# Kernel optimization log

Hardware: AMD Instinct MI355X
Metric: run time of the kernel (lower is better)

Reference implementation:

```python
import jax, jax.numpy as jnp
import numpy as np

B, P = 512, 256          # batch, n_assets
MAX_W = 0.1              # max_weight from __init__
EPS = 1e-8               # config.EPSILON
N_PGD = 250              # projected-gradient iterations (QP solve)
N_BISECT = 30            # bisection iterations for simplex projection
N_POWER = 20             # power iterations for spectral norm


def setup_inputs() -> dict:
    key = jax.random.key(0)
    k1, k2 = jax.random.split(key, 2)
    A = jax.random.normal(k1, (B, P, P), jnp.float32)
    # PSD covariance, as required by cp.Parameter(PSD=True)
    sigma = jnp.einsum('bij,bkj->bik', A, A) / P + 1e-3 * jnp.eye(P, dtype=jnp.float32)
    beta = jax.random.uniform(k2, (B, P), jnp.float32)  # nonneg risk budgets
    w_prev = jnp.full((B, P), 1.0 / P, jnp.float32)     # default equal weight
    return {
        'sigma': sigma,
        'beta': beta,
        'w_prev': w_prev,
        'log_lambda1': jnp.float32(-3.0),
        'log_lambda2': jnp.float32(-2.0),
    }


def _project_capped_simplex(v, c):
    """Euclidean projection onto {w : sum w = 1, 0 <= w <= c}, batched over leading dims.
    Solves sum(clip(v - tau, 0, c)) = 1 for tau by bisection (monotone decreasing)."""
    lo = v.min(-1, keepdims=True) - c
    hi = v.max(-1, keepdims=True)

    def body(i, carry):
        lo, hi = carry
        tau = 0.5 * (lo + hi)
        s = jnp.clip(v - tau, 0.0, c).sum(-1, keepdims=True)
        too_big = s > 1.0
        return (jnp.where(too_big, tau, lo), jnp.where(too_big, hi, tau))

    lo, hi = jax.lax.fori_loop(0, N_BISECT, body, (lo, hi))
    tau = 0.5 * (lo + hi)
    return jnp.clip(v - tau, 0.0, c)


def _solve_qp(sigma, beta, w_prev, lam1, lam2):
    """min_w  w'Pw - beta'w + lam1*||w||_1 + lam2*||w - w_prev||^2
       s.t.   sum w = 1, 0 <= w <= MAX_W
    via projected gradient descent (on the feasible set w>=0, ||w||_1 = sum w,
    so lam1 contributes a constant lam1 to the gradient)."""
    # step size 1/L with L = 2*lambda_max(P) + 2*lam2, estimated by power iteration
    S = jax.lax.stop_gradient(sigma)
    v = jnp.full((B, P), 1.0 / np.sqrt(P), sigma.dtype)

    def pbody(i, v):
        u = jnp.einsum('bij,bj->bi', S, v)
        return u / (jnp.linalg.norm(u, axis=-1, keepdims=True) + EPS)

    v = jax.lax.fori_loop(0, N_POWER, pbody, v)
    lmax = jnp.einsum('bi,bij,bj->b', v, S, v)                    # [B]
    step = jax.lax.stop_gradient(1.0 / (2.0 * lmax + 2.0 * lam2 + 1e-6))  # [B]

    w0 = jnp.full((B, P), 1.0 / P, sigma.dtype)

    def pgd(w, _):
        g = (2.0 * jnp.einsum('bij,bj->bi', sigma, w)
             - beta + lam1 + 2.0 * lam2 * (w - w_prev))
        w = _project_capped_simplex(w - step[:, None] * g, MAX_W)
        return w, None

    w, _ = jax.lax.scan(pgd, w0, None, length=N_PGD)
    return w


def reference(sigma, beta, w_prev, log_lambda1, log_lambda2):
    lam1 = jnp.exp(log_lambda1)
    lam2 = jnp.exp(log_lambda2)
    w = _solve_qp(sigma, beta, w_prev, lam1, lam2)
    # post-processing from forward(): clamp then renormalize
    w = jnp.clip(w, 0.0, MAX_W)
    return w / (w.sum(-1, keepdims=True) + EPS)
```

## Files before the change

### kernel.cpp

```cpp
#include <hip/hip_runtime.h>
#include <math.h>


#define PP    256
#define MAXW  0.1f
#define EPSF  1e-8f
#define NPGD  250
#define NPOW  20
#define NILLMAX 10
#define FTOL  4e-6f
#define STOPTOL 1e-7f
#define MINIT 48

#define R3S   272
#define TJS   68
#define WRDS  72
#define VCOPY 280

typedef float v2 __attribute__((ext_vector_type(2)));
typedef float v4t __attribute__((ext_vector_type(4)));

template<int CTRL>
__device__ __forceinline__ float dpp_zero(float x) {
    return __int_as_float(__builtin_amdgcn_update_dpp(
        0, __float_as_int(x), CTRL, 0xF, 0xF, true));
}
template<int CTRL>
__device__ __forceinline__ float dpp_keep(float x) {
    int xi = __float_as_int(x);
    return __int_as_float(__builtin_amdgcn_update_dpp(xi, xi, CTRL, 0xF, 0xF, false));
}
__device__ __forceinline__ float rdlane63(float x) {
    return __int_as_float(__builtin_amdgcn_readlane(__float_as_int(x), 63));
}
__device__ __forceinline__ float wave_sum63(float s) {
    s += dpp_zero<0x111>(s);
    s += dpp_zero<0x112>(s);
    s += dpp_zero<0x114>(s);
    s += dpp_zero<0x118>(s);
    s += dpp_zero<0x142>(s);
    s += dpp_zero<0x143>(s);
    return s;
}
__device__ __forceinline__ float wave_min63(float m) {
    m = fminf(m, dpp_keep<0x111>(m));
    m = fminf(m, dpp_keep<0x112>(m));
    m = fminf(m, dpp_keep<0x114>(m));
    m = fminf(m, dpp_keep<0x118>(m));
    m = fminf(m, dpp_keep<0x142>(m));
    m = fminf(m, dpp_keep<0x143>(m));
    return m;
}
__device__ __forceinline__ float wave_max63(float m) {
    m = fmaxf(m, dpp_keep<0x111>(m));
    m = fmaxf(m, dpp_keep<0x112>(m));
    m = fmaxf(m, dpp_keep<0x114>(m));
    m = fmaxf(m, dpp_keep<0x118>(m));
    m = fmaxf(m, dpp_keep<0x142>(m));
    m = fmaxf(m, dpp_keep<0x143>(m));
    return m;
}

__global__ __launch_bounds__(256, 2)
__attribute__((amdgpu_waves_per_eu(2, 2)))
void drb_kernel(const float* __restrict__ sigma,
                const float* __restrict__ beta,
                const float* __restrict__ wprev,
                const float* __restrict__ pl1,
                const float* __restrict__ pl2,
                float* __restrict__ out)
{
    const int b    = blockIdx.x;
    const int tid  = threadIdx.x;
    const int lane = tid & 63;
    const int wv   = tid >> 6;
    const int ti   = tid >> 2;
    const int tj   = tid & 3;

    __shared__ __align__(16) float sigR3[64 * R3S];
    __shared__ __align__(16) float wcop[4 * VCOPY];
    __shared__ __align__(16) float stage[2][256];

    const float* Sb = sigma + (size_t)b * (PP * PP);

    v2 s0[32], s1[32], s2[32];
    {
        const float* r0 = Sb + (4 * ti + 0) * PP + 64 * tj;
#pragma unroll
        for (int k = 0; k < 16; ++k) {
            v4t t = *(const v4t*)(r0 + 4 * k);
            s0[2*k]   = __builtin_shufflevector(t, t, 0, 1);
            s0[2*k+1] = __builtin_shufflevector(t, t, 2, 3);
        }
    }
    {
        const float* r1 = Sb + (4 * ti + 1) * PP + 64 * tj;
#pragma unroll
        for (int k = 0; k < 16; ++k) {
            v4t t = *(const v4t*)(r1 + 4 * k);
            s1[2*k]   = __builtin_shufflevector(t, t, 0, 1);
            s1[2*k+1] = __builtin_shufflevector(t, t, 2, 3);
        }
    }
    {
        const float* r2 = Sb + (4 * ti + 2) * PP + 64 * tj;
#pragma unroll
        for (int k = 0; k < 16; ++k) {
            v4t t = *(const v4t*)(r2 + 4 * k);
            s2[2*k]   = __builtin_shufflevector(t, t, 0, 1);
            s2[2*k+1] = __builtin_shufflevector(t, t, 2, 3);
        }
    }
    {
        const float* r3 = Sb + (4 * ti + 3) * PP + 64 * tj;
        float* d3 = sigR3 + ti * R3S + TJS * tj;
#pragma unroll
        for (int k = 0; k < 16; ++k)
            *(v4t*)(d3 + 4 * k) = *(const v4t*)(r3 + 4 * k);
    }

    const float bt   = beta[b * PP + tid];
    const float wp   = wprev[b * PP + tid];
    const float lam1 = expf(pl1[0]);
    const float lam2 = expf(pl2[0]);

    float* wme = wcop + wv * VCOPY;
    const int wst = 4 * lane + 8 * (lane >> 4);
    const float* wrd = wme + WRDS * tj;

    auto matvec = [&]() -> float {
        v2 y0a = {0.f, 0.f}, y0b = {0.f, 0.f};
        v2 y1a = {0.f, 0.f}, y1b = {0.f, 0.f};
        v2 y2a = {0.f, 0.f}, y2b = {0.f, 0.f};
        v2 y3a = {0.f, 0.f}, y3b = {0.f, 0.f};
        const float* p3 = sigR3 + ti * R3S + TJS * tj;
#pragma unroll
        for (int k = 0; k < 16; ++k) {
            v4t wq = *(const v4t*)(wrd + 4 * k);
            v2 w01 = __builtin_shufflevector(wq, wq, 0, 1);
            v2 w23 = __builtin_shufflevector(wq, wq, 2, 3);
            y0a = __builtin_elementwise_fma(s0[2*k],   w01, y0a);
            y0b = __builtin_elementwise_fma(s0[2*k+1], w23, y0b);
            y1a = __builtin_elementwise_fma(s1[2*k],   w01, y1a);
            y1b = __builtin_elementwise_fma(s1[2*k+1], w23, y1b);
            y2a = __builtin_elementwise_fma(s2[2*k],   w01, y2a);
            y2b = __builtin_elementwise_fma(s2[2*k+1], w23, y2b);
            v4t q = *(const v4t*)(p3 + 4 * k);
            v2 q01 = __builtin_shufflevector(q, q, 0, 1);
            v2 q23 = __builtin_shufflevector(q, q, 2, 3);
            y3a = __builtin_elementwise_fma(q01, w01, y3a);
            y3b = __builtin_elementwise_fma(q23, w23, y3b);
        }
        float r0 = (y0a.x + y0a.y) + (y0b.x + y0b.y);
        float r1 = (y1a.x + y1a.y) + (y1b.x + y1b.y);
        float r2 = (y2a.x + y2a.y) + (y2b.x + y2b.y);
        float r3 = (y3a.x + y3a.y) + (y3b.x + y3b.y);
        r0 += dpp_zero<0x4E>(r0); r1 += dpp_zero<0x4E>(r1);
        r2 += dpp_zero<0x4E>(r2); r3 += dpp_zero<0x4E>(r3);
        r0 += dpp_zero<0xB1>(r0); r1 += dpp_zero<0xB1>(r1);
        r2 += dpp_zero<0xB1>(r2); r3 += dpp_zero<0xB1>(r3);
        float a01 = (tj & 1) ? r1 : r0;
        float a23 = (tj & 1) ? r3 : r2;
        return (tj & 2) ? a23 : a01;
    };

    {
        v4t c = {0.0625f, 0.0625f, 0.0625f, 0.0625f};
        *(v4t*)(wme + wst) = c;
    }

    float y_last = 0.f, a_last = 1.f;
#pragma unroll 1
    for (int pi = 0; pi < NPOW; ++pi) {
        float y = matvec();
        stage[pi & 1][tid] = y;
        __syncthreads();
        v4t u4 = *(const v4t*)(&stage[pi & 1][4 * lane]);
        float ss = fmaf(u4.x, u4.x, fmaf(u4.y, u4.y, fmaf(u4.z, u4.z, u4.w * u4.w)));
        float a  = 1.f / (sqrtf(rdlane63(wave_sum63(ss))) + EPSF);
        v4t n4 = {a * u4.x, a * u4.y, a * u4.z, a * u4.w};
        *(v4t*)(wme + wst) = n4;
        y_last = y; a_last = a;
    }

    float stepf;
    {
        float ysv = matvec();
        float p   = (a_last * y_last) * ysv;
        stage[0][tid] = p;
        __syncthreads();
        v4t p4 = *(const v4t*)(&stage[0][4 * lane]);
        float lmax = rdlane63(wave_sum63((p4.x + p4.y) + (p4.z + p4.w)));
        stepf = 1.f / (2.f * lmax + 2.f * lam2 + 1e-6f);
        __syncthreads();
    }

    float w_own = 1.f / 256.f;
    {
        v4t c = {1.f/256.f, 1.f/256.f, 1.f/256.f, 1.f/256.f};
        *(v4t*)(wme + wst) = c;
    }
    const float Ac = 1.f - 2.f * lam2 * stepf;
    const float Bc = -2.f * stepf;
    const float Cc = stepf * (bt - lam1 + 2.f * lam2 * wp);

    float tau_pred = 0.f;
    float tau_last = 0.f;
    float dtau_last = 0.f;

    v4t w4_prev = {1.f/256.f, 1.f/256.f, 1.f/256.f, 1.f/256.f};
    float dm1 = 1.f, dm2 = 1.f;

#pragma unroll 1
    for (int it = 0; it < NPGD; ++it) {
        if (it >= MINIT && dm1 < STOPTOL && dm2 < STOPTOL) break;

        float y = matvec();
        float v_own = fmaf(w_own, Ac, fmaf(y, Bc, Cc));
        const int sb = it & 1;
        stage[sb][tid] = v_own;
        __syncthreads();

        __builtin_amdgcn_s_setprio(1);
        v4t v4 = *(const v4t*)(&stage[sb][4 * lane]);

        float tau = tau_pred;
        {
            float d0 = v4.x - tau, d1 = v4.y - tau;
            float d2 = v4.z - tau, d3 = v4.w - tau;
            float c0 = __builtin_amdgcn_fmed3f(d0, 0.f, MAXW);
            float c1 = __builtin_amdgcn_fmed3f(d1, 0.f, MAXW);
            float c2 = __builtin_amdgcn_fmed3f(d2, 0.f, MAXW);
            float c3 = __builtin_amdgcn_fmed3f(d3, 0.f, MAXW);
            float Sw = wave_sum63((c0 + c1) + (c2 + c3));
            float f  = rdlane63(Sw) - 1.f;

            if (!(fabsf(f) <= FTOL)) {
                float mnl = fminf(fminf(v4.x, v4.y), fminf(v4.z, v4.w));
                float mxl = fmaxf(fmaxf(v4.x, v4.y), fmaxf(v4.z, v4.w));
                float n0 = ((d0 > 0.f) & (d0 < MAXW)) ? 1.f : 0.f;
                float n1 = ((d1 > 0.f) & (d1 < MAXW)) ? 1.f : 0.f;
                float n2 = ((d2 > 0.f) & (d2 < MAXW)) ? 1.f : 0.f;
                float n3 = ((d3 > 0.f) & (d3 < MAXW)) ? 1.f : 0.f;
                float mnw = wave_min63(mnl);
                float mxw = wave_max63(mxl);
                float Nw  = wave_sum63((n0 + n1) + (n2 + n3));
                float mn  = rdlane63(mnw);
                float mx  = rdlane63(mxw);
                float cnt = rdlane63(Nw);
                bool pos0 = f > 0.f;
                float lo  = pos0 ? tau : mn - MAXW;
                float flo = pos0 ? f   : 256.f * MAXW - 1.f;
                float hi  = pos0 ? mx  : tau;
                float fhi = pos0 ? -1.f : f;
                int side  = pos0 ? 1 : -1;
#pragma unroll 1
                for (int r = 1; r < NILLMAX; ++r) {
                    float tn = fmaf(f, __builtin_amdgcn_rcpf(cnt), tau);
                    float ts = (lo * fhi - hi * flo) *
                               __builtin_amdgcn_rcpf(fhi - flo);
                    bool good = (tn > lo) & (tn < hi);
                    tau = good ? tn : ts;
                    float e0 = v4.x - tau, e1 = v4.y - tau;
                    float e2 = v4.z - tau, e3 = v4.w - tau;
                    float g0 = __builtin_amdgcn_fmed3f(e0, 0.f, MAXW);
                    float g1 = __builtin_amdgcn_fmed3f(e1, 0.f, MAXW);
                    float g2 = __builtin_amdgcn_fmed3f(e2, 0.f, MAXW);
                    float g3 = __builtin_amdgcn_fmed3f(e3, 0.f, MAXW);
                    float m0 = ((e0 > 0.f) & (e0 < MAXW)) ? 1.f : 0.f;
                    float m1 = ((e1 > 0.f) & (e1 < MAXW)) ? 1.f : 0.f;
                    float m2 = ((e2 > 0.f) & (e2 < MAXW)) ? 1.f : 0.f;
                    float m3 = ((e3 > 0.f) & (e3 < MAXW)) ? 1.f : 0.f;
                    float Sr = wave_sum63((g0 + g1) + (g2 + g3));
                    float Nr = wave_sum63((m0 + m1) + (m2 + m3));
                    f   = rdlane63(Sr) - 1.f;
                    cnt = rdlane63(Nr);
                    if (fabsf(f) <= FTOL) break;
                    bool pos = f > 0.f;
                    float nflo = pos ? f   : ((side < 0) ? 0.5f * flo : flo);
                    float nfhi = pos ? ((side > 0) ? 0.5f * fhi : fhi) : f;
                    lo  = pos ? tau : lo;
                    hi  = pos ? hi  : tau;
                    flo = nflo; fhi = nfhi;
                    side = pos ? 1 : -1;
                }
            }
        }

        {
            float dtau = tau - tau_last;
            float rho  = dtau * __builtin_amdgcn_rcpf(dtau_last);
            bool okx = (fabsf(dtau_last) > 1e-20f) & (rho > 0.f) &
                       (rho < 0.9f) & (fabsf(dtau) < 1e-2f);
            float extr = okx ? dtau * rho * __builtin_amdgcn_rcpf(1.f - rho) : 0.f;
            tau_pred = tau + extr;
            tau_last = tau;
            dtau_last = dtau;
        }

        v4t w4 = {__builtin_amdgcn_fmed3f(v4.x - tau, 0.f, MAXW),
                  __builtin_amdgcn_fmed3f(v4.y - tau, 0.f, MAXW),
                  __builtin_amdgcn_fmed3f(v4.z - tau, 0.f, MAXW),
                  __builtin_amdgcn_fmed3f(v4.w - tau, 0.f, MAXW)};
        *(v4t*)(wme + wst) = w4;
        __builtin_amdgcn_s_setprio(0);
        w_own = __builtin_amdgcn_fmed3f(v_own - tau, 0.f, MAXW);

        {
            float pm = fmaxf(fmaxf(fabsf(w4.x - w4_prev.x),
                                   fabsf(w4.y - w4_prev.y)),
                             fmaxf(fabsf(w4.z - w4_prev.z),
                                   fabsf(w4.w - w4_prev.w)));
            w4_prev = w4;
            dm2 = dm1;
            dm1 = rdlane63(wave_max63(pm));
        }
    }

    __syncthreads();
    stage[0][tid] = w_own;
    __syncthreads();
    v4t w4 = *(const v4t*)(&stage[0][4 * lane]);
    float S = rdlane63(wave_sum63((w4.x + w4.y) + (w4.z + w4.w)));
    out[b * PP + tid] = w_own / (S + EPSF);
}

extern "C" void kernel_launch(void* const* d_in, const int* in_sizes, int n_in,
                              void* d_out, int out_size, void* d_ws, size_t ws_size,
                              hipStream_t stream) {
    const float* sigma  = (const float*)d_in[0];
    const float* beta   = (const float*)d_in[1];
    const float* wprevp = (const float*)d_in[2];
    const float* pl1    = (const float*)d_in[3];
    const float* pl2    = (const float*)d_in[4];
    float* outp = (float*)d_out;
    drb_kernel<<<dim3(512), dim3(256), 0, stream>>>(sigma, beta, wprevp, pl1, pl2, outp);
}
```

Measured before the change: 330.2 us.

## Add strongly-convex heavy-ball momentum to projected gradient QP solver

Replaces plain projected gradient descent with an accelerated variant. The gradient is now evaluated at an extrapolated point z = w + b*(w - w_prev), with the momentum coefficient derived from the condition ratio sqrt(mu/L). The step size uses a 1.15 safety factor on L, and momentum is switched off when the update magnitude grows, as an adaptive restart. The minimum iteration count before the convergence-based early exit drops from 48 to 24. The aim is to converge to the same minimizer in far fewer matvec iterations. The risk is that the iterate trajectory and the stopping point differ from the fixed 250-step reference, which could affect tolerance.

```diff
diff --git a/kernel.cpp b/kernel.cpp
--- a/kernel.cpp
+++ b/kernel.cpp
@@ -10,7 +10,7 @@
 #define NILLMAX 10
 #define FTOL  4e-6f
 #define STOPTOL 1e-7f
-#define MINIT 48
+#define MINIT 24
 
 #define R3S   272
 #define TJS   68
@@ -183,7 +183,7 @@
         y_last = y; a_last = a;
     }
 
-    float stepf;
+    float stepf, bmom;
     {
         float ysv = matvec();
         float p   = (a_last * y_last) * ysv;
@@ -191,11 +191,16 @@
         __syncthreads();
         v4t p4 = *(const v4t*)(&stage[0][4 * lane]);
         float lmax = rdlane63(wave_sum63((p4.x + p4.y) + (p4.z + p4.w)));
-        stepf = 1.f / (2.f * lmax + 2.f * lam2 + 1e-6f);
+        float Lsafe = 1.15f * (2.f * lmax + 2.f * lam2) + 1e-6f;
+        stepf = 1.f / Lsafe;
+        float mu = 2.f * lam2 + 2e-3f;
+        float q  = sqrtf(mu / Lsafe);
+        bmom = (1.f - q) / (1.f + q);
         __syncthreads();
     }
 
     float w_own = 1.f / 256.f;
+    float z_own = 1.f / 256.f;
     {
         v4t c = {1.f/256.f, 1.f/256.f, 1.f/256.f, 1.f/256.f};
         *(v4t*)(wme + wst) = c;
@@ -214,9 +219,10 @@
 #pragma unroll 1
     for (int it = 0; it < NPGD; ++it) {
         if (it >= MINIT && dm1 < STOPTOL && dm2 < STOPTOL) break;
+        const float bm = (dm1 > 1.2f * dm2) ? 0.f : bmom;
 
         float y = matvec();
-        float v_own = fmaf(w_own, Ac, fmaf(y, Bc, Cc));
+        float v_own = fmaf(z_own, Ac, fmaf(y, Bc, Cc));
         const int sb = it & 1;
         stage[sb][tid] = v_own;
         __syncthreads();
@@ -298,20 +304,26 @@
             dtau_last = dtau;
         }
 
-        v4t w4 = {__builtin_amdgcn_fmed3f(v4.x - tau, 0.f, MAXW),
-                  __builtin_amdgcn_fmed3f(v4.y - tau, 0.f, MAXW),
-                  __builtin_amdgcn_fmed3f(v4.z - tau, 0.f, MAXW),
-                  __builtin_amdgcn_fmed3f(v4.w - tau, 0.f, MAXW)};
-        *(v4t*)(wme + wst) = w4;
+        v4t w4n = {__builtin_amdgcn_fmed3f(v4.x - tau, 0.f, MAXW),
+                   __builtin_amdgcn_fmed3f(v4.y - tau, 0.f, MAXW),
+                   __builtin_amdgcn_fmed3f(v4.z - tau, 0.f, MAXW),
+                   __builtin_amdgcn_fmed3f(v4.w - tau, 0.f, MAXW)};
+        v4t z4 = {fmaf(bm, w4n.x - w4_prev.x, w4n.x),
+                  fmaf(bm, w4n.y - w4_prev.y, w4n.y),
+                  fmaf(bm, w4n.z - w4_prev.z, w4n.z),
+                  fmaf(bm, w4n.w - w4_prev.w, w4n.w)};
+        *(v4t*)(wme + wst) = z4;
         __builtin_amdgcn_s_setprio(0);
-        w_own = __builtin_amdgcn_fmed3f(v_own - tau, 0.f, MAXW);
+        float w_new = __builtin_amdgcn_fmed3f(v_own - tau, 0.f, MAXW);
+        z_own = fmaf(bm, w_new - w_own, w_new);
+        w_own = w_new;
 
         {
-            float pm = fmaxf(fmaxf(fabsf(w4.x - w4_prev.x),
-                                   fabsf(w4.y - w4_prev.y)),
-                             fmaxf(fabsf(w4.z - w4_prev.z),
-                                   fabsf(w4.w - w4_prev.w)));
-            w4_prev = w4;
+            float pm = fmaxf(fmaxf(fabsf(w4n.x - w4_prev.x),
+                                   fabsf(w4n.y - w4_prev.y)),
+                             fmaxf(fabsf(w4n.z - w4_prev.z),
+                                   fabsf(w4n.w - w4_prev.w)));
+            w4_prev = w4n;
             dm2 = dm1;
             dm1 = rdlane63(wave_max63(pm));
         }
```

Result: faster. 304.3 us (-7.9%).
